# Optimization experiments

Measured on AMD Instinct MI355X. Metric: run time of the kernel, lower is better.

The kernel has to match this reference:

```python
import jax, jax.numpy as jnp
import numpy as np

N = 100000          # num_nodes
OUT = 64            # out_channels
E = 3200000         # num edges (avg degree 32)


def setup_inputs() -> dict:
    key = jax.random.key(0)
    k1, k2, k3 = jax.random.split(key, 3)
    edge_index = jax.random.randint(k1, (2, E), 0, N, dtype=jnp.int64)
    # nn.Linear(num_nodes, out_channels): W is [out, in] = [OUT, N]
    bound = 1.0 / np.sqrt(N)
    W = jax.random.uniform(k2, (OUT, N), jnp.float32, -bound, bound)
    b = jax.random.uniform(k3, (OUT,), jnp.float32, -bound, bound)
    return {"edge_index": edge_index, "W": W, "b": b}


def reference(edge_index, W, b):
    # LINK forward: A = sparse COO adjacency (N x N, value 1 per edge,
    # duplicates accumulate), logits = A @ W.T + b.
    # Row i of A @ W.T = sum over edges (i -> j) of W[:, j].
    row, col = edge_index[0], edge_index[1]
    msgs = W.T[col]                                  # [E, OUT] gather of W columns
    logits = jax.ops.segment_sum(msgs, row, num_segments=N)  # [N, OUT]
    return logits + b
```

## Files before the change

kernel.cpp:

```cpp
#include <hip/hip_runtime.h>
#include <hip/hip_bf16.h>


#define OUTC 64
#define NFX  2048
#define SLAB 2560
#define SCOLN (SLAB + 256)
#define EPB  12544
#define PT   1024
#define GT   512

__device__ inline unsigned f2bf(float x) {
    unsigned u = __float_as_uint(x);
    return (u + 0x7FFFu + ((u >> 16) & 1u)) >> 16;
}
__device__ inline float bf_lo(unsigned u) { return __uint_as_float(u << 16); }
__device__ inline float bf_hi(unsigned u) { return __uint_as_float(u & 0xFFFF0000u); }

__global__ __launch_bounds__(PT) void part_trans(const int* __restrict__ rows,
                                                 const int* __restrict__ cols,
                                                 const float* __restrict__ W,
                                                 unsigned* __restrict__ WTh,
                                                 int* __restrict__ gcur,
                                                 unsigned* __restrict__ packed,
                                                 int E, int N, int NF) {
    __shared__ union {
        float tile[64][65];
        struct {
            unsigned lbuf[EPB];
            int cnt[NFX];
            int loff[NFX + 1];
            int lcur[NFX];
            int gbase[NFX];
            int partial[PT];
        } p1;
    } sh;
    const int tid = threadIdx.x;

    const int ntiles = (N + 63) >> 6;
    for (int t = blockIdx.x; t < ntiles; t += gridDim.x) {
        const int n0 = t * 64;
        {
            int o = tid >> 4, q = tid & 15;
            int nn = n0 + q * 4;
            if (nn + 3 < N) {
                float4 v = *(const float4*)(W + (size_t)o * N + nn);
                sh.tile[o][q * 4 + 0] = v.x;
                sh.tile[o][q * 4 + 1] = v.y;
                sh.tile[o][q * 4 + 2] = v.z;
                sh.tile[o][q * 4 + 3] = v.w;
            } else {
                for (int j = 0; j < 4; ++j)
                    sh.tile[o][q * 4 + j] = (nn + j < N) ? W[(size_t)o * N + nn + j] : 0.f;
            }
        }
        __syncthreads();
        #pragma unroll
        for (int k2 = 0; k2 < 2; ++k2) {
            int idx = tid + k2 * PT;
            int nl = idx >> 5, u = idx & 31;
            int nn = n0 + nl;
            if (nn < N)
                WTh[(size_t)nn * 32 + u] =
                    f2bf(sh.tile[2 * u][nl]) | (f2bf(sh.tile[2 * u + 1][nl]) << 16);
        }
        __syncthreads();
    }

    const int nchunks = (E + EPB - 1) / EPB;
    for (int c = blockIdx.x; c < nchunks; c += gridDim.x) {
        const int base = c * EPB;
        const int lim  = min(E, base + EPB);
        const int nE   = lim - base;

        for (int i = tid; i < NFX; i += PT) sh.p1.cnt[i] = 0;
        __syncthreads();

        for (int e = base + tid * 4; e + 3 < lim; e += PT * 4) {
            int4 r = *(const int4*)(rows + e);
            atomicAdd(&sh.p1.cnt[r.x >> 6], 1);
            atomicAdd(&sh.p1.cnt[r.y >> 6], 1);
            atomicAdd(&sh.p1.cnt[r.z >> 6], 1);
            atomicAdd(&sh.p1.cnt[r.w >> 6], 1);
        }
        {
            int ts = base + (nE & ~3);
            for (int e = ts + tid; e < lim; e += PT)
                atomicAdd(&sh.p1.cnt[rows[e] >> 6], 1);
        }
        __syncthreads();

        int v0 = sh.p1.cnt[2 * tid], v1 = sh.p1.cnt[2 * tid + 1];
        int s  = v0 + v1;
        sh.p1.partial[tid] = s;
        __syncthreads();
        for (int off = 1; off < PT; off <<= 1) {
            int t = 0;
            if (tid >= off) t = sh.p1.partial[tid - off];
            __syncthreads();
            if (tid >= off) sh.p1.partial[tid] += t;
            __syncthreads();
        }
        int ex = sh.p1.partial[tid] - s;
        sh.p1.loff[2 * tid]     = ex;
        sh.p1.loff[2 * tid + 1] = ex + v0;
        sh.p1.lcur[2 * tid]     = ex;
        sh.p1.lcur[2 * tid + 1] = ex + v0;
        if (tid == PT - 1) sh.p1.loff[NFX] = sh.p1.partial[PT - 1];
        __syncthreads();

        for (int b = tid; b < NF; b += PT) {
            int cc = sh.p1.cnt[b];
            sh.p1.gbase[b] = b * SLAB + (cc ? atomicAdd(&gcur[b], cc) : 0);
        }
        __syncthreads();

        for (int e = base + tid * 4; e + 3 < lim; e += PT * 4) {
            int4 r  = *(const int4*)(rows + e);
            int4 cc = *(const int4*)(cols + e);
            int p0 = atomicAdd(&sh.p1.lcur[r.x >> 6], 1);
            int p1 = atomicAdd(&sh.p1.lcur[r.y >> 6], 1);
            int p2 = atomicAdd(&sh.p1.lcur[r.z >> 6], 1);
            int p3 = atomicAdd(&sh.p1.lcur[r.w >> 6], 1);
            sh.p1.lbuf[p0] = ((unsigned)(r.x & 63) << 17) | (unsigned)cc.x;
            sh.p1.lbuf[p1] = ((unsigned)(r.y & 63) << 17) | (unsigned)cc.y;
            sh.p1.lbuf[p2] = ((unsigned)(r.z & 63) << 17) | (unsigned)cc.z;
            sh.p1.lbuf[p3] = ((unsigned)(r.w & 63) << 17) | (unsigned)cc.w;
        }
        {
            int ts = base + (nE & ~3);
            for (int e = ts + tid; e < lim; e += PT) {
                int r = rows[e];
                int p = atomicAdd(&sh.p1.lcur[r >> 6], 1);
                sh.p1.lbuf[p] = ((unsigned)(r & 63) << 17) | (unsigned)cols[e];
            }
        }
        __syncthreads();

        const int chunk = (nE + PT - 1) / PT;
        int i0 = tid * chunk;
        int i1 = min(nE, i0 + chunk);
        if (i0 < i1) {
            int lo = 0, hi = NFX;
            while (hi - lo > 1) {
                int mid = (lo + hi) >> 1;
                if (sh.p1.loff[mid] <= i0) lo = mid; else hi = mid;
            }
            int b = lo;
            for (int i = i0; i < i1; ++i) {
                while (i >= sh.p1.loff[b + 1]) ++b;
                int pos = sh.p1.gbase[b] + (i - sh.p1.loff[b]);
                if (pos < (b + 1) * SLAB)
                    packed[pos] = sh.p1.lbuf[i];
            }
        }
        __syncthreads();
    }
}

__global__ __launch_bounds__(GT) void sort_gather3(const unsigned* __restrict__ WTh,
                                                   const unsigned* __restrict__ packed,
                                                   const int* __restrict__ gcur,
                                                   const float* __restrict__ bias,
                                                   float* __restrict__ out, int N) {
    __shared__ __align__(16) unsigned scol[SCOLN];
    __shared__ int cw[8 * 64];
    __shared__ int off0[64], tend[64];
    const int b    = blockIdx.x;
    const int tid  = threadIdx.x;
    const int lane = tid & 63;
    const int w    = tid >> 6;
    const int start = b * SLAB;
    int size = gcur[b];
    if (size > SLAB) size = SLAB;

    cw[tid] = 0;
    for (int i = tid; i < SCOLN; i += GT) scol[i] = 0u;
    __syncthreads();

    for (int e = tid; e < size; e += GT)
        atomicAdd(&cw[w * 64 + (packed[start + e] >> 17)], 1);
    __syncthreads();

    if (tid < 64) {
        int c0 = cw[tid],        c1 = cw[64 + tid],  c2 = cw[128 + tid], c3 = cw[192 + tid];
        int c4 = cw[256 + tid],  c5 = cw[320 + tid], c6 = cw[384 + tid], c7 = cw[448 + tid];
        int v  = c0 + c1 + c2 + c3 + c4 + c5 + c6 + c7;
        int va = (v + 3) & ~3;
        int inc = va;
        #pragma unroll
        for (int d = 1; d < 64; d <<= 1) {
            int t = __shfl_up(inc, d, 64);
            if (lane >= d) inc += t;
        }
        int ex = inc - va;
        off0[tid] = ex;
        tend[tid] = ex + v;
        int run = ex;
        cw[tid]       = run; run += c0;
        cw[64 + tid]  = run; run += c1;
        cw[128 + tid] = run; run += c2;
        cw[192 + tid] = run; run += c3;
        cw[256 + tid] = run; run += c4;
        cw[320 + tid] = run; run += c5;
        cw[384 + tid] = run; run += c6;
        cw[448 + tid] = run;
    }
    __syncthreads();

    for (int e = tid; e < size; e += GT) {
        unsigned u = packed[start + e];
        int p = atomicAdd(&cw[w * 64 + (u >> 17)], 1);
        scol[p] = u & 0x1FFFFu;
    }
    __syncthreads();

    const int g = tid >> 3;
    const int q = tid & 7;
    const unsigned* Wq = WTh + q * 4;
    const float4 bv0 = *(const float4*)(bias + q * 8);
    const float4 bv1 = *(const float4*)(bias + q * 8 + 4);
    const int s = off0[g];
    const int t = tend[g];
    float a0 = 0.f, a1 = 0.f, a2 = 0.f, a3 = 0.f;
    float a4 = 0.f, a5 = 0.f, a6 = 0.f, a7 = 0.f;

    int mx = t - s;
    #pragma unroll
    for (int d = 8; d < 64; d <<= 1) {
        int o = __shfl_xor(mx, d, 64);
        mx = mx > o ? mx : o;
    }

    int e = s;
    for (int it = (mx + 3) >> 2; it > 0; --it, e += 4) {
        if (e < t) {
            uint4 cc = *(const uint4*)(scol + e);
            uint4 u0 = *(const uint4*)(Wq + ((size_t)(cc.x << 5)));
            uint4 u1 = *(const uint4*)(Wq + ((size_t)(cc.y << 5)));
            uint4 u2 = *(const uint4*)(Wq + ((size_t)(cc.z << 5)));
            uint4 u3 = *(const uint4*)(Wq + ((size_t)(cc.w << 5)));
            float m1 = (e + 1 < t) ? 1.f : 0.f;
            float m2 = (e + 2 < t) ? 1.f : 0.f;
            float m3 = (e + 3 < t) ? 1.f : 0.f;
            a0 += bf_lo(u0.x); a1 += bf_hi(u0.x);
            a2 += bf_lo(u0.y); a3 += bf_hi(u0.y);
            a4 += bf_lo(u0.z); a5 += bf_hi(u0.z);
            a6 += bf_lo(u0.w); a7 += bf_hi(u0.w);
            a0 = fmaf(m1, bf_lo(u1.x), a0); a1 = fmaf(m1, bf_hi(u1.x), a1);
            a2 = fmaf(m1, bf_lo(u1.y), a2); a3 = fmaf(m1, bf_hi(u1.y), a3);
            a4 = fmaf(m1, bf_lo(u1.z), a4); a5 = fmaf(m1, bf_hi(u1.z), a5);
            a6 = fmaf(m1, bf_lo(u1.w), a6); a7 = fmaf(m1, bf_hi(u1.w), a7);
            a0 = fmaf(m2, bf_lo(u2.x), a0); a1 = fmaf(m2, bf_hi(u2.x), a1);
            a2 = fmaf(m2, bf_lo(u2.y), a2); a3 = fmaf(m2, bf_hi(u2.y), a3);
            a4 = fmaf(m2, bf_lo(u2.z), a4); a5 = fmaf(m2, bf_hi(u2.z), a5);
            a6 = fmaf(m2, bf_lo(u2.w), a6); a7 = fmaf(m2, bf_hi(u2.w), a7);
            a0 = fmaf(m3, bf_lo(u3.x), a0); a1 = fmaf(m3, bf_hi(u3.x), a1);
            a2 = fmaf(m3, bf_lo(u3.y), a2); a3 = fmaf(m3, bf_hi(u3.y), a3);
            a4 = fmaf(m3, bf_lo(u3.z), a4); a5 = fmaf(m3, bf_hi(u3.z), a5);
            a6 = fmaf(m3, bf_lo(u3.w), a6); a7 = fmaf(m3, bf_hi(u3.w), a7);
        }
    }

    const int n = b * 64 + g;
    if (n < N) {
        float4 o1, o2;
        o1.x = a0 + bv0.x; o1.y = a1 + bv0.y; o1.z = a2 + bv0.z; o1.w = a3 + bv0.w;
        o2.x = a4 + bv1.x; o2.y = a5 + bv1.y; o2.z = a6 + bv1.z; o2.w = a7 + bv1.w;
        *(float4*)(out + (size_t)n * 64 + q * 8)     = o1;
        *(float4*)(out + (size_t)n * 64 + q * 8 + 4) = o2;
    }
}

extern "C" void kernel_launch(void* const* d_in, const int* in_sizes, int n_in,
                              void* d_out, int out_size, void* d_ws, size_t ws_size,
                              hipStream_t stream) {
    const int*   edges = (const int*)d_in[0];
    const float* W     = (const float*)d_in[1];
    const float* bias  = (const float*)d_in[2];
    float*       out   = (float*)d_out;

    const int E  = in_sizes[0] / 2;
    const int N  = in_sizes[1] / OUTC;
    const int NF = (N + 63) / 64;

    char* ws = (char*)d_ws;
    size_t off = 0;
    unsigned* WTh = (unsigned*)(ws + off); off += (size_t)N * 32 * sizeof(unsigned);
    off = (off + 255) & ~(size_t)255;
    int* gcur = (int*)(ws + off);          off += (size_t)NF * sizeof(int);
    off = (off + 255) & ~(size_t)255;
    unsigned* packed = (unsigned*)(ws + off); off += (size_t)NF * SLAB * sizeof(unsigned);
    (void)ws_size;

    const int* rows = edges;
    const int* cols = edges + E;

    hipMemsetAsync(gcur, 0, (size_t)NF * sizeof(int), stream);
    part_trans<<<256, PT, 0, stream>>>(rows, cols, W, WTh, gcur, packed, E, N, NF);
    sort_gather3<<<NF, GT, 0, stream>>>(WTh, packed, gcur, bias, out, N);
}
```

Measured before the change: 175.4 us.

## Split sort and gather kernels, quarter-channel WT layout for cache locality

Splits the fused sort+gather kernel into a per-slab sort kernel that writes sorted columns and offsets back to global memory, and a separate gather kernel. The transposed bf16 W is re-laid out so each channel quarter of the table is contiguous (N×16 channels). The gather grid is grouped by quarter so concurrently running blocks hit a smaller working set in L2/MALL. The aim is better cache hit rate for the random row gathers, at the cost of an extra kernel launch, a global round-trip of the sorted columns, and four passes over the column lists. The sort kernel also caps slab size at SLAB-192 instead of SLAB.

```diff
diff --git a/kernel.cpp b/kernel.cpp
--- a/kernel.cpp
+++ b/kernel.cpp
@@ -5,10 +5,11 @@
 #define OUTC 64
 #define NFX  2048
 #define SLAB 2560
-#define SCOLN (SLAB + 256)
 #define EPB  12544
 #define PT   1024
-#define GT   512
+
+typedef unsigned u32x4v __attribute__((ext_vector_type(4)));
+typedef float    f32x4v __attribute__((ext_vector_type(4)));
 
 __device__ inline unsigned f2bf(float x) {
     unsigned u = __float_as_uint(x);
@@ -61,7 +62,7 @@
             int nl = idx >> 5, u = idx & 31;
             int nn = n0 + nl;
             if (nn < N)
-                WTh[(size_t)nn * 32 + u] =
+                WTh[((size_t)(u >> 3) * N + nn) * 8 + (u & 7)] =
                     f2bf(sh.tile[2 * u][nl]) | (f2bf(sh.tile[2 * u + 1][nl]) << 16);
         }
         __syncthreads();
@@ -158,27 +159,26 @@
     }
 }
 
-__global__ __launch_bounds__(GT) void sort_gather3(const unsigned* __restrict__ WTh,
-                                                   const unsigned* __restrict__ packed,
-                                                   const int* __restrict__ gcur,
-                                                   const float* __restrict__ bias,
-                                                   float* __restrict__ out, int N) {
-    __shared__ __align__(16) unsigned scol[SCOLN];
+__global__ __launch_bounds__(512) void sortk(unsigned* __restrict__ packed,
+                                             const int* __restrict__ gcur,
+                                             int* __restrict__ offs) {
+    __shared__ __align__(16) unsigned scol[SLAB];
     __shared__ int cw[8 * 64];
     __shared__ int off0[64], tend[64];
+    __shared__ int padtot;
     const int b    = blockIdx.x;
     const int tid  = threadIdx.x;
     const int lane = tid & 63;
     const int w    = tid >> 6;
     const int start = b * SLAB;
     int size = gcur[b];
-    if (size > SLAB) size = SLAB;
+    if (size > SLAB - 192) size = SLAB - 192;
 
     cw[tid] = 0;
-    for (int i = tid; i < SCOLN; i += GT) scol[i] = 0u;
+    for (int i = tid; i < SLAB; i += 512) scol[i] = 0u;
     __syncthreads();
 
-    for (int e = tid; e < size; e += GT)
+    for (int e = tid; e < size; e += 512)
         atomicAdd(&cw[w * 64 + (packed[start + e] >> 17)], 1);
     __syncthreads();
 
@@ -196,6 +196,7 @@
         int ex = inc - va;
         off0[tid] = ex;
         tend[tid] = ex + v;
+        if (tid == 63) padtot = inc;
         int run = ex;
         cw[tid]       = run; run += c0;
         cw[64 + tid]  = run; run += c1;
@@ -208,38 +209,56 @@
     }
     __syncthreads();
 
-    for (int e = tid; e < size; e += GT) {
+    for (int e = tid; e < size; e += 512) {
         unsigned u = packed[start + e];
         int p = atomicAdd(&cw[w * 64 + (u >> 17)], 1);
         scol[p] = u & 0x1FFFFu;
     }
     __syncthreads();
 
-    const int g = tid >> 3;
-    const int q = tid & 7;
-    const unsigned* Wq = WTh + q * 4;
-    const float4 bv0 = *(const float4*)(bias + q * 8);
-    const float4 bv1 = *(const float4*)(bias + q * 8 + 4);
-    const int s = off0[g];
-    const int t = tend[g];
+    const int pt = padtot;
+    for (int i = tid; i < pt; i += 512) packed[start + i] = scol[i];
+    if (tid < 128) offs[b * 128 + tid] = (tid < 64) ? off0[tid] : tend[tid - 64];
+}
+
+__global__ __launch_bounds__(256) void gatherq(const unsigned* __restrict__ WThQ,
+                                               const unsigned* __restrict__ scols,
+                                               const int* __restrict__ offs,
+                                               const float* __restrict__ bias,
+                                               float* __restrict__ out, int N, int NF) {
+    const int i       = blockIdx.x;
+    const int quarter = (i & 7) >> 1;
+    const int j       = ((i >> 3) << 1) | (i & 1);
+    if (j >= NF) return;
+    const int tid = threadIdx.x;
+    const int q2  = tid & 1;
+    const int h   = (tid >> 1) & 1;
+    const int g   = tid >> 2;
+
+    const int s = offs[j * 128 + g];
+    const int t = offs[j * 128 + 64 + g];
+    const unsigned* Wq = WThQ + (size_t)quarter * N * 8 + q2 * 4;
+    const unsigned* sc = scols + (size_t)j * SLAB;
+
     float a0 = 0.f, a1 = 0.f, a2 = 0.f, a3 = 0.f;
     float a4 = 0.f, a5 = 0.f, a6 = 0.f, a7 = 0.f;
 
-    int mx = t - s;
+    int e = s + h * 4;
+    int trips = (t > e) ? ((t - e + 7) >> 3) : 0;
+    int mx = trips;
     #pragma unroll
-    for (int d = 8; d < 64; d <<= 1) {
+    for (int d = 1; d < 64; d <<= 1) {
         int o = __shfl_xor(mx, d, 64);
         mx = mx > o ? mx : o;
     }
 
-    int e = s;
-    for (int it = (mx + 3) >> 2; it > 0; --it, e += 4) {
+    for (int it = mx; it > 0; --it, e += 8) {
         if (e < t) {
-            uint4 cc = *(const uint4*)(scol + e);
-            uint4 u0 = *(const uint4*)(Wq + ((size_t)(cc.x << 5)));
-            uint4 u1 = *(const uint4*)(Wq + ((size_t)(cc.y << 5)));
-            uint4 u2 = *(const uint4*)(Wq + ((size_t)(cc.z << 5)));
-            uint4 u3 = *(const uint4*)(Wq + ((size_t)(cc.w << 5)));
+            u32x4v cc = __builtin_nontemporal_load((const u32x4v*)(sc + e));
+            uint4 u0 = *(const uint4*)(Wq + (size_t)cc.x * 8);
+            uint4 u1 = *(const uint4*)(Wq + (size_t)cc.y * 8);
+            uint4 u2 = *(const uint4*)(Wq + (size_t)cc.z * 8);
+            uint4 u3 = *(const uint4*)(Wq + (size_t)cc.w * 8);
             float m1 = (e + 1 < t) ? 1.f : 0.f;
             float m2 = (e + 2 < t) ? 1.f : 0.f;
             float m3 = (e + 3 < t) ? 1.f : 0.f;
@@ -262,13 +281,23 @@
         }
     }
 
-    const int n = b * 64 + g;
-    if (n < N) {
-        float4 o1, o2;
-        o1.x = a0 + bv0.x; o1.y = a1 + bv0.y; o1.z = a2 + bv0.z; o1.w = a3 + bv0.w;
-        o2.x = a4 + bv1.x; o2.y = a5 + bv1.y; o2.z = a6 + bv1.z; o2.w = a7 + bv1.w;
-        *(float4*)(out + (size_t)n * 64 + q * 8)     = o1;
-        *(float4*)(out + (size_t)n * 64 + q * 8 + 4) = o2;
+    a0 += __shfl_xor(a0, 2, 64); a1 += __shfl_xor(a1, 2, 64);
+    a2 += __shfl_xor(a2, 2, 64); a3 += __shfl_xor(a3, 2, 64);
+    a4 += __shfl_xor(a4, 2, 64); a5 += __shfl_xor(a5, 2, 64);
+    a6 += __shfl_xor(a6, 2, 64); a7 += __shfl_xor(a7, 2, 64);
+
+    if (h == 0) {
+        const int n = j * 64 + g;
+        if (n < N) {
+            const int ch = quarter * 16 + q2 * 8;
+            const float4 bv0 = *(const float4*)(bias + ch);
+            const float4 bv1 = *(const float4*)(bias + ch + 4);
+            f32x4v o1, o2;
+            o1.x = a0 + bv0.x; o1.y = a1 + bv0.y; o1.z = a2 + bv0.z; o1.w = a3 + bv0.w;
+            o2.x = a4 + bv1.x; o2.y = a5 + bv1.y; o2.z = a6 + bv1.z; o2.w = a7 + bv1.w;
+            __builtin_nontemporal_store(o1, (f32x4v*)(out + (size_t)n * 64 + ch));
+            __builtin_nontemporal_store(o2, (f32x4v*)(out + (size_t)n * 64 + ch + 4));
+        }
     }
 }
 
@@ -286,17 +315,22 @@
 
     char* ws = (char*)d_ws;
     size_t off = 0;
-    unsigned* WTh = (unsigned*)(ws + off); off += (size_t)N * 32 * sizeof(unsigned);
+    unsigned* WThQ = (unsigned*)(ws + off); off += (size_t)N * 32 * sizeof(unsigned);
     off = (off + 255) & ~(size_t)255;
     int* gcur = (int*)(ws + off);          off += (size_t)NF * sizeof(int);
     off = (off + 255) & ~(size_t)255;
     unsigned* packed = (unsigned*)(ws + off); off += (size_t)NF * SLAB * sizeof(unsigned);
+    off = (off + 255) & ~(size_t)255;
+    int* offs = (int*)(ws + off);          off += (size_t)NF * 128 * sizeof(int);
     (void)ws_size;
 
     const int* rows = edges;
     const int* cols = edges + E;
 
+    const int NB2 = (NF + 1) & ~1;
+
     hipMemsetAsync(gcur, 0, (size_t)NF * sizeof(int), stream);
-    part_trans<<<256, PT, 0, stream>>>(rows, cols, W, WTh, gcur, packed, E, N, NF);
-    sort_gather3<<<NF, GT, 0, stream>>>(WTh, packed, gcur, bias, out, N);
-}
+    part_trans<<<256, PT, 0, stream>>>(rows, cols, W, WThQ, gcur, packed, E, N, NF);
+    sortk<<<NF, 512, 0, stream>>>(packed, gcur, offs);
+    gatherq<<<4 * NB2, 256, 0, stream>>>(WThQ, packed, offs, bias, out, N, NF);
+}
```

Result: slower. 237.5 us (+35.4%).
